# Kernel optimization log

Hardware: AMD Instinct MI355X
Metric: run time of the kernel (lower is better)

The kernel has to match this reference:

```python
import jax, jax.numpy as jnp
import numpy as np

IMAGE_SIZE = 224


def setup_inputs() -> dict:
    key = jax.random.key(0)
    ks = jax.random.split(key, 8)
    B, N = 8, 200
    return {
        "z": jax.random.normal(ks[0], (B, 512), jnp.float32),
        "z_lib": jax.random.normal(ks[1], (N, 512), jnp.float32),
        "fmap0": jax.random.normal(ks[2], (B, 64, 56, 56), jnp.float32),
        "fmap1": jax.random.normal(ks[3], (B, 128, 28, 28), jnp.float32),
        "fmap2": jax.random.normal(ks[4], (B, 256, 14, 14), jnp.float32),
        "lib0": jax.random.normal(ks[5], (N, 64, 56, 56), jnp.float32),
        "lib1": jax.random.normal(ks[6], (N, 128, 28, 28), jnp.float32),
        "lib2": jax.random.normal(ks[7], (N, 256, 14, 14), jnp.float32),
        "k": 5,
    }


def reference(z, z_lib, fmap0, fmap1, fmap2, lib0, lib1, lib2, k):
    B = z.shape[0]
    # Pairwise Euclidean distances [B, N] (equivalent to the nested-loop cdist)
    d2 = (jnp.sum(z * z, axis=1)[:, None]
          + jnp.sum(z_lib * z_lib, axis=1)[None, :]
          - 2.0 * z @ z_lib.T)
    dist = jnp.sqrt(jnp.maximum(d2, 0.0))
    # top-k smallest distances
    neg_vals, idx = jax.lax.top_k(-dist, k)  # [B, k]
    values = -neg_vals
    z_score = values.mean(axis=-1).reshape(-1, 1)  # [B, 1]

    scaled_s_map = jnp.zeros((B, 1, IMAGE_SIZE, IMAGE_SIZE), dist.dtype)
    for fmap, lib in ((fmap0, lib0), (fmap1, lib1), (fmap2, lib2)):
        nearest = lib[idx]  # [B, k, C, H, W] gather of nearest train fmaps
        # fused squared-diff -> sum over channels -> min over k neighbors
        s_map = jnp.min(jnp.sum((nearest - fmap[:, None]) ** 2, axis=2), axis=1)  # [B, H, W]
        up = jax.image.resize(s_map[:, None], (B, 1, IMAGE_SIZE, IMAGE_SIZE), method="bilinear")
        scaled_s_map = scaled_s_map + up
    return (z_score, scaled_s_map)
```

## Files before the change

### kernel.cpp

```cpp
#include <hip/hip_runtime.h>
#include <cfloat>

#define KK 5
#define BB 8
#define NN 200
#define DD 512
#define MAGIC 0x5AFE0000u
#define P2_UNITS 644

__device__ __forceinline__ unsigned long long umin64(unsigned long long a,
                                                     unsigned long long b)
{ return b < a ? b : a; }

__device__ __forceinline__ unsigned fkey(float v) {
    unsigned u = __float_as_uint(v);
    return (u & 0x80000000u) ? ~u : (u | 0x80000000u);
}
__device__ __forceinline__ float fkey_inv(unsigned k) {
    return __uint_as_float((k & 0x80000000u) ? (k ^ 0x80000000u) : ~k);
}

template <int C, int HW>
__device__ __forceinline__ void smap_store(
    const float* __restrict__ fmap, const float* __restrict__ lib,
    const int* idxl, float* __restrict__ sm, int gid)
{
    if (gid >= KK * BB * HW) return;
    int px = gid % HW;
    int r  = gid / HW;
    int b  = r % BB;
    int k  = r / BB;
    int id = idxl[b * KK + k];

    const float* f = fmap + (size_t)b  * C * HW + px;
    const float* l = lib  + (size_t)id * C * HW + px;

    float acc = 0.f;
#pragma unroll 16
    for (int c = 0; c < C; ++c) {
        float d = l[(size_t)c * HW] - f[(size_t)c * HW];
        acc = fmaf(d, d, acc);
    }
    sm[(size_t)(k * BB + b) * HW + px] = acc;
}

__global__ __launch_bounds__(256) void fused_ab(
    const float* __restrict__ z, const float* __restrict__ zlib,
    const float* __restrict__ fmap0, const float* __restrict__ fmap1,
    const float* __restrict__ fmap2,
    const float* __restrict__ lib0, const float* __restrict__ lib1,
    const float* __restrict__ lib2,
    float* __restrict__ out, unsigned* __restrict__ widx_g,
    float* __restrict__ sm0, float* __restrict__ sm1, float* __restrict__ sm2)
{
    const int tid = threadIdx.x;
    const int blk = blockIdx.x;

    if (blk < BB) {
        __shared__ float4 zs4[DD / 4];
        __shared__ float  dist[256];
        if (tid < DD / 4)
            zs4[tid] = ((const float4*)(z + (size_t)blk * DD))[tid];
        __syncthreads();

        {
            float ll = 0.f, dot = 0.f;
            if (tid < NN) {
                const float4* lrow = (const float4*)(zlib + (size_t)tid * DD);
#pragma unroll 8
                for (int c = 0; c < DD / 4; ++c) {
                    float4 l = lrow[c];
                    float4 a = zs4[c];
                    ll  = fmaf(l.x, l.x, fmaf(l.y, l.y,
                          fmaf(l.z, l.z, fmaf(l.w, l.w, ll))));
                    dot = fmaf(l.x, a.x, fmaf(l.y, a.y,
                          fmaf(l.z, a.z, fmaf(l.w, a.w, dot))));
                }
            }
            dist[tid] = (tid < NN) ? (ll - 2.f * dot) : FLT_MAX;
        }
        __syncthreads();

        if (tid < 64) {
            const float4* zb4 = (const float4*)(z + (size_t)blk * DD);
            float4 a = zb4[tid], c2 = zb4[tid + 64];
            float zz = a.x*a.x + a.y*a.y + a.z*a.z + a.w*a.w
                     + c2.x*c2.x + c2.y*c2.y + c2.z*c2.z + c2.w*c2.w;
#pragma unroll
            for (int m = 32; m; m >>= 1) zz += __shfl_xor(zz, m);

            unsigned long long pk[4];
#pragma unroll
            for (int j = 0; j < 4; ++j) {
                int n = tid + 64 * j;
                pk[j] = ((unsigned long long)fkey(dist[n]) << 32) | (unsigned)n;
            }
            float sum = 0.f;
            for (int r = 0; r < KK; ++r) {
                unsigned long long p = umin64(umin64(pk[0], pk[1]),
                                              umin64(pk[2], pk[3]));
#pragma unroll
                for (int m = 32; m; m >>= 1)
                    p = umin64(p, __shfl_xor(p, m));
                unsigned widx = (unsigned)(p & 0xFFFFFFFFu);
                sum += sqrtf(fmaxf(zz + fkey_inv((unsigned)(p >> 32)), 0.f));
                if (tid == 0)
                    __hip_atomic_store(&widx_g[blk * KK + r], MAGIC | widx,
                                       __ATOMIC_RELAXED,
                                       __HIP_MEMORY_SCOPE_AGENT);
#pragma unroll
                for (int j = 0; j < 4; ++j)
                    if ((unsigned)(pk[j] & 0xFFFFFFFFu) == widx)
                        pk[j] = 0xFFFFFFFFFFFFFFFFull;
            }
            if (tid == 0) out[blk] = sum * (1.f / KK);
        }
        return;
    }

    __shared__ int sidx[BB * KK];
    if (tid < BB * KK) {
        unsigned v;
        do {
            v = __hip_atomic_load(&widx_g[tid], __ATOMIC_RELAXED,
                                  __HIP_MEMORY_SCOPE_AGENT);
        } while ((v & 0xFFFF0000u) != MAGIC);
        sidx[tid] = (int)(v & 0xFFFFu);
    }
    __syncthreads();

    int u = blk - BB;
    if (u < 490) {
        smap_store<64, 3136>(fmap0, lib0, sidx, sm0, u * 256 + tid);
    } else if (u < 613) {
        smap_store<128, 784>(fmap1, lib1, sidx, sm1, (u - 490) * 256 + tid);
    } else {
        smap_store<256, 196>(fmap2, lib2, sidx, sm2, (u - 613) * 256 + tid);
    }
}

template <int S, int HW>
__device__ __forceinline__ float tap_min(const float* __restrict__ sm, int b,
                                         int yx)
{
    float m = FLT_MAX;
#pragma unroll
    for (int k = 0; k < KK; ++k)
        m = fminf(m, sm[(size_t)(k * BB + b) * HW + yx]);
    return m;
}

template <int S, int HW>
__device__ __forceinline__ float bil5(const float* __restrict__ sm, int b,
                                      int oy, int ox)
{
    const float scale = (float)S * (1.f / 224.f);
    float sy = fminf(fmaxf((oy + 0.5f) * scale - 0.5f, 0.f), (float)(S - 1));
    float sx = fminf(fmaxf((ox + 0.5f) * scale - 0.5f, 0.f), (float)(S - 1));
    int y0 = (int)sy, x0 = (int)sx;
    float ty = sy - y0, tx = sx - x0;
    int y1 = min(y0 + 1, S - 1), x1 = min(x0 + 1, S - 1);
    float v00 = tap_min<S, HW>(sm, b, y0 * S + x0);
    float v01 = tap_min<S, HW>(sm, b, y0 * S + x1);
    float v10 = tap_min<S, HW>(sm, b, y1 * S + x0);
    float v11 = tap_min<S, HW>(sm, b, y1 * S + x1);
    float top = v00 + tx * (v01 - v00);
    float bot = v10 + tx * (v11 - v10);
    return top + ty * (bot - top);
}

__global__ __launch_bounds__(256) void upsample_kernel(
    const float* __restrict__ sm0, const float* __restrict__ sm1,
    const float* __restrict__ sm2, float* __restrict__ out)
{
    int gid = blockIdx.x * 256 + threadIdx.x;
    if (gid >= BB * 224 * 224) return;
    int ox = gid % 224;
    int r  = gid / 224;
    int oy = r % 224;
    int b  = r / 224;

    float v = bil5<56, 3136>(sm0, b, oy, ox)
            + bil5<28,  784>(sm1, b, oy, ox)
            + bil5<14,  196>(sm2, b, oy, ox);
    out[BB + gid] = v;
}

extern "C" void kernel_launch(void* const* d_in, const int* in_sizes, int n_in,
                              void* d_out, int out_size, void* d_ws, size_t ws_size,
                              hipStream_t stream)
{
    const float* z     = (const float*)d_in[0];
    const float* zlib  = (const float*)d_in[1];
    const float* fmap0 = (const float*)d_in[2];
    const float* fmap1 = (const float*)d_in[3];
    const float* fmap2 = (const float*)d_in[4];
    const float* lib0  = (const float*)d_in[5];
    const float* lib1  = (const float*)d_in[6];
    const float* lib2  = (const float*)d_in[7];
    float* out = (float*)d_out;

    char* ws = (char*)d_ws;
    unsigned* widx = (unsigned*)ws;
    float* sm0 = (float*)(ws + 256);
    float* sm1 = sm0 + (size_t)KK * BB * 3136;
    float* sm2 = sm1 + (size_t)KK * BB * 784;

    fused_ab<<<BB + P2_UNITS, 256, 0, stream>>>(z, zlib,
                                                fmap0, fmap1, fmap2,
                                                lib0, lib1, lib2,
                                                out, widx, sm0, sm1, sm2);

    upsample_kernel<<<1568, 256, 0, stream>>>(sm0, sm1, sm2, out);
}
```

Baseline: 36.43 us.

## Fuse upsample into main kernel via grid-wide flag barrier

```diff
diff --git a/kernel.cpp b/kernel.cpp
--- a/kernel.cpp
+++ b/kernel.cpp
@@ -5,8 +5,10 @@
 #define BB 8
 #define NN 200
 #define DD 512
-#define MAGIC 0x5AFE0000u
+#define MAGIC  0x5AFE0000u
+#define FMAGIC 0x5AFEF00Du
 #define P2_UNITS 644
+#define P3_UNITS 1568
 
 __device__ __forceinline__ unsigned long long umin64(unsigned long long a,
                                                      unsigned long long b)
@@ -44,13 +46,44 @@
     sm[(size_t)(k * BB + b) * HW + px] = acc;
 }
 
-__global__ __launch_bounds__(256) void fused_ab(
+template <int S, int HW>
+__device__ __forceinline__ float tap_min(const float* __restrict__ sm, int b,
+                                         int yx)
+{
+    float m = FLT_MAX;
+#pragma unroll
+    for (int k = 0; k < KK; ++k)
+        m = fminf(m, sm[(size_t)(k * BB + b) * HW + yx]);
+    return m;
+}
+
+template <int S, int HW>
+__device__ __forceinline__ float bil5(const float* __restrict__ sm, int b,
+                                      int oy, int ox)
+{
+    const float scale = (float)S * (1.f / 224.f);
+    float sy = fminf(fmaxf((oy + 0.5f) * scale - 0.5f, 0.f), (float)(S - 1));
+    float sx = fminf(fmaxf((ox + 0.5f) * scale - 0.5f, 0.f), (float)(S - 1));
+    int y0 = (int)sy, x0 = (int)sx;
+    float ty = sy - y0, tx = sx - x0;
+    int y1 = min(y0 + 1, S - 1), x1 = min(x0 + 1, S - 1);
+    float v00 = tap_min<S, HW>(sm, b, y0 * S + x0);
+    float v01 = tap_min<S, HW>(sm, b, y0 * S + x1);
+    float v10 = tap_min<S, HW>(sm, b, y1 * S + x0);
+    float v11 = tap_min<S, HW>(sm, b, y1 * S + x1);
+    float top = v00 + tx * (v01 - v00);
+    float bot = v10 + tx * (v11 - v10);
+    return top + ty * (bot - top);
+}
+
+__global__ __launch_bounds__(256) void spade_one(
     const float* __restrict__ z, const float* __restrict__ zlib,
     const float* __restrict__ fmap0, const float* __restrict__ fmap1,
     const float* __restrict__ fmap2,
     const float* __restrict__ lib0, const float* __restrict__ lib1,
     const float* __restrict__ lib2,
-    float* __restrict__ out, unsigned* __restrict__ widx_g,
+    float* __restrict__ out,
+    unsigned* __restrict__ widx_g, unsigned* __restrict__ flags,
     float* __restrict__ sm0, float* __restrict__ sm1, float* __restrict__ sm2)
 {
     const int tid = threadIdx.x;
@@ -129,7 +162,7 @@
     }
     __syncthreads();
 
-    int u = blk - BB;
+    const int u = blk - BB;
     if (u < 490) {
         smap_store<64, 3136>(fmap0, lib0, sidx, sm0, u * 256 + tid);
     } else if (u < 613) {
@@ -137,53 +170,36 @@
     } else {
         smap_store<256, 196>(fmap2, lib2, sidx, sm2, (u - 613) * 256 + tid);
     }
-}
-
-template <int S, int HW>
-__device__ __forceinline__ float tap_min(const float* __restrict__ sm, int b,
-                                         int yx)
-{
-    float m = FLT_MAX;
-#pragma unroll
-    for (int k = 0; k < KK; ++k)
-        m = fminf(m, sm[(size_t)(k * BB + b) * HW + yx]);
-    return m;
-}
-
-template <int S, int HW>
-__device__ __forceinline__ float bil5(const float* __restrict__ sm, int b,
-                                      int oy, int ox)
-{
-    const float scale = (float)S * (1.f / 224.f);
-    float sy = fminf(fmaxf((oy + 0.5f) * scale - 0.5f, 0.f), (float)(S - 1));
-    float sx = fminf(fmaxf((ox + 0.5f) * scale - 0.5f, 0.f), (float)(S - 1));
-    int y0 = (int)sy, x0 = (int)sx;
-    float ty = sy - y0, tx = sx - x0;
-    int y1 = min(y0 + 1, S - 1), x1 = min(x0 + 1, S - 1);
-    float v00 = tap_min<S, HW>(sm, b, y0 * S + x0);
-    float v01 = tap_min<S, HW>(sm, b, y0 * S + x1);
-    float v10 = tap_min<S, HW>(sm, b, y1 * S + x0);
-    float v11 = tap_min<S, HW>(sm, b, y1 * S + x1);
-    float top = v00 + tx * (v01 - v00);
-    float bot = v10 + tx * (v11 - v10);
-    return top + ty * (bot - top);
-}
-
-__global__ __launch_bounds__(256) void upsample_kernel(
-    const float* __restrict__ sm0, const float* __restrict__ sm1,
-    const float* __restrict__ sm2, float* __restrict__ out)
-{
-    int gid = blockIdx.x * 256 + threadIdx.x;
-    if (gid >= BB * 224 * 224) return;
-    int ox = gid % 224;
-    int r  = gid / 224;
-    int oy = r % 224;
-    int b  = r / 224;
-
-    float v = bil5<56, 3136>(sm0, b, oy, ox)
-            + bil5<28,  784>(sm1, b, oy, ox)
-            + bil5<14,  196>(sm2, b, oy, ox);
-    out[BB + gid] = v;
+
+    __syncthreads();
+    if (tid == 0)
+        __hip_atomic_store(&flags[u], FMAGIC, __ATOMIC_RELEASE,
+                           __HIP_MEMORY_SCOPE_AGENT);
+
+    if (tid < 161) {
+#pragma unroll
+        for (int j = 0; j < 4; ++j) {
+            int f = tid * 4 + j;
+            if (f < P2_UNITS) {
+                while (__hip_atomic_load(&flags[f], __ATOMIC_ACQUIRE,
+                                         __HIP_MEMORY_SCOPE_AGENT) != FMAGIC)
+                    __builtin_amdgcn_s_sleep(2);
+            }
+        }
+    }
+    __syncthreads();
+
+    for (int w = u; w < P3_UNITS; w += P2_UNITS) {
+        int gid = w * 256 + tid;
+        int ox = gid % 224;
+        int r  = gid / 224;
+        int oy = r % 224;
+        int b  = r / 224;
+        float v = bil5<56, 3136>(sm0, b, oy, ox)
+                + bil5<28,  784>(sm1, b, oy, ox)
+                + bil5<14,  196>(sm2, b, oy, ox);
+        out[BB + gid] = v;
+    }
 }
 
 extern "C" void kernel_launch(void* const* d_in, const int* in_sizes, int n_in,
@@ -201,15 +217,15 @@
     float* out = (float*)d_out;
 
     char* ws = (char*)d_ws;
-    unsigned* widx = (unsigned*)ws;
-    float* sm0 = (float*)(ws + 256);
+    unsigned* widx  = (unsigned*)ws;
+    unsigned* flags = widx + 64;
+    float* sm0 = (float*)(ws + 4096);
     float* sm1 = sm0 + (size_t)KK * BB * 3136;
     float* sm2 = sm1 + (size_t)KK * BB * 784;
 
-    fused_ab<<<BB + P2_UNITS, 256, 0, stream>>>(z, zlib,
-                                                fmap0, fmap1, fmap2,
-                                                lib0, lib1, lib2,
-                                                out, widx, sm0, sm1, sm2);
-
-    upsample_kernel<<<1568, 256, 0, stream>>>(sm0, sm1, sm2, out);
-}
+    spade_one<<<BB + P2_UNITS, 256, 0, stream>>>(z, zlib,
+                                                 fmap0, fmap1, fmap2,
+                                                 lib0, lib1, lib2,
+                                                 out, widx, flags,
+                                                 sm0, sm1, sm2);
+}
```

Measured after the change: 97.75 us. 2.68x slower.
